# Optimization experiments

Hardware: AMD Instinct MI355X
Metric: run time of the kernel (lower is better)

## Reference

```python
import jax, jax.numpy as jnp
import numpy as np

EPS = 1e-6

def _layernorm2d(x, w, b):
    # normalize over channel dim (axis=1) per (b,h,w)
    u = jnp.mean(x, axis=1, keepdims=True)
    s = jnp.mean((x - u) ** 2, axis=1, keepdims=True)
    xn = (x - u) / jnp.sqrt(s + EPS)
    return xn * w[None, :, None, None] + b[None, :, None, None]

def _conv1x1(x, w, b):
    # w: (O, C, 1, 1)
    y = jnp.einsum('bchw,oc->bohw', x, w[:, :, 0, 0])
    return y + b[None, :, None, None]

def _dwconv3x3(x, w):
    # w: (C, 1, 3, 3), groups = C, padding 1, no bias
    C = x.shape[1]
    return jax.lax.conv_general_dilated(
        x, w, window_strides=(1, 1), padding=((1, 1), (1, 1)),
        dimension_numbers=('NCHW', 'OIHW', 'NCHW'), feature_group_count=C)

def _linrec_scan(a, u, axis):
    # s_t = a_t * s_{t-1} + u_t via associative scan
    def comb(l, r):
        al, ul = l
        ar, ur = r
        return al * ar, ar * ul + ur
    return jax.lax.associative_scan(comb, (a, u), axis=axis)[1]

def _bidir_scan(z, a, b, g, axis):
    u = b * z
    s_f = _linrec_scan(a, u, axis)
    s_b = jnp.flip(_linrec_scan(jnp.flip(a, axis), jnp.flip(u, axis), axis), axis)
    return g * (s_f + s_b)

def setup_inputs() -> dict:
    key = jax.random.key(0)
    ks = jax.random.split(key, 6)
    B, C, H, W = 8, 192, 128, 128
    x = jax.random.normal(ks[0], (B, C, H, W), dtype=jnp.float32)
    ln_w = jnp.ones((C,), jnp.float32)
    ln_b = jnp.zeros((C,), jnp.float32)
    dw_w = jax.random.normal(ks[1], (C, 1, 3, 3), jnp.float32) * (1.0 / 3.0)
    loc_w = jax.random.normal(ks[2], (C, C, 1, 1), jnp.float32) * (1.0 / np.sqrt(C))
    loc_b = jnp.zeros((C,), jnp.float32)
    par_w = jax.random.normal(ks[3], (3 * C, C, 1, 1), jnp.float32) * (1.0 / np.sqrt(C))
    par_b = jnp.zeros((3 * C,), jnp.float32)
    out_w = jax.random.normal(ks[4], (C, C, 1, 1), jnp.float32) * (1.0 / np.sqrt(C))
    out_b = jnp.zeros((C,), jnp.float32)
    return {"x": x, "ln_w": ln_w, "ln_b": ln_b, "dw_w": dw_w,
            "loc_w": loc_w, "loc_b": loc_b, "par_w": par_w, "par_b": par_b,
            "out_w": out_w, "out_b": out_b}

def reference(x, ln_w, ln_b, dw_w, loc_w, loc_b, par_w, par_b, out_w, out_b):
    C = x.shape[1]
    z = _layernorm2d(x, ln_w, ln_b)
    local_feat = _conv1x1(_dwconv3x3(z, dw_w), loc_w, loc_b)
    gates = _conv1x1(z, par_w, par_b)
    alpha = jax.nn.sigmoid(gates[:, :C])
    beta = jax.nn.sigmoid(gates[:, C:2 * C])
    gamma = jax.nn.sigmoid(gates[:, 2 * C:])
    y_w = _bidir_scan(z, alpha, beta, gamma, axis=3)  # along W
    y_h = _bidir_scan(z, alpha, beta, gamma, axis=2)  # along H
    y = local_feat + 0.5 * (y_w + y_h)
    y = jax.nn.silu(y)
    y = _conv1x1(y, out_w, out_b)
    return x + y
```

## Files before the change

### kernel.cpp

```cpp
#include <hip/hip_runtime.h>
#include <cstdint>
#include <cstddef>

#define B 8
#define C 192
#define H 128
#define W 128
#define HW (H * W)
#define CHW ((size_t)C * HW)
#define K C

typedef __attribute__((ext_vector_type(8))) short short8v;
typedef __attribute__((ext_vector_type(4))) float f32x4;
typedef __attribute__((ext_vector_type(4))) unsigned short ushort4v;

__device__ __forceinline__ float bf2f(unsigned short s) {
    union { float f; unsigned u; } cv; cv.u = ((unsigned)s) << 16; return cv.f;
}
__device__ __forceinline__ unsigned short f2bf(float f) {
    union { float f; unsigned u; } cv; cv.f = f;
    unsigned r = (cv.u + 0x7fffu + ((cv.u >> 16) & 1u)) >> 16;
    return (unsigned short)r;
}

__global__ void prepack_kernel(const float* __restrict__ pw, const float* __restrict__ lw,
                               const float* __restrict__ ow, unsigned short* __restrict__ wb) {
    int i = blockIdx.x * 256 + threadIdx.x;
    const int NPW = 3 * C * K, NL = C * K;
    if (i < NPW) wb[i] = f2bf(pw[i]);
    else if (i < NPW + NL) wb[i] = f2bf(lw[i - NPW]);
    else if (i < NPW + 2 * NL) wb[i] = f2bf(ow[i - NPW - NL]);
}

__global__ void ln_kernel(const float* __restrict__ x, const float* __restrict__ lw,
                          const float* __restrict__ lb, unsigned short* __restrict__ zt,
                          unsigned short* __restrict__ zn) {
    int p = blockIdx.x * 256 + threadIdx.x;
    int b = p >> 14, hw = p & 16383;
    const float* xp = x + (size_t)b * CHW + hw;
    float sum = 0.f, sq = 0.f;
    for (int c = 0; c < C; ++c) {
        float v = xp[(size_t)c * HW];
        sum += v; sq += v * v;
    }
    float mean = sum * (1.0f / C);
    float var = fmaxf(sq * (1.0f / C) - mean * mean, 0.f);
    float rs = rsqrtf(var + 1e-6f);
    unsigned short* zp = zt + (size_t)p * K;
    unsigned short* znp = zn + (size_t)b * CHW + hw;
#pragma unroll 4
    for (int c8 = 0; c8 < K / 8; ++c8) {
        short8v v;
#pragma unroll
        for (int j = 0; j < 8; ++j) {
            int c = c8 * 8 + j;
            float r = (xp[(size_t)c * HW] - mean) * rs * lw[c] + lb[c];
            unsigned short rb = f2bf(r);
            v[j] = (short)rb;
            znp[(size_t)c * HW] = rb;
        }
        *(short8v*)(zp + c8 * 8) = v;
    }
}

template <int MODE>
__global__ __launch_bounds__(256, 4)
void conv_mfma_kernel(const unsigned short* __restrict__ zt, const unsigned short* __restrict__ yin,
                      const unsigned short* __restrict__ zn,
                      const unsigned short* __restrict__ wb, const float* __restrict__ bias,
                      const float* __restrict__ xres, float* __restrict__ Pf,
                      unsigned short* __restrict__ PA, unsigned short* __restrict__ PU,
                      unsigned short* __restrict__ PG) {
    __shared__ char smem[96 * 384];
    int tid = threadIdx.x;
    int lane = tid & 63, wv = tid >> 6;
    int p0 = blockIdx.x * 128 + wv * 32;
    int lr = lane & 15, lh = lane >> 4;
    int sw = (lr & 7) << 4;

    short8v bfr[2][6];
    if (MODE != 2) {
#pragma unroll
        for (int s = 0; s < 2; ++s) {
            const unsigned short* zr = zt + (size_t)(p0 + s * 16 + lr) * K + lh * 8;
#pragma unroll
            for (int t = 0; t < 6; ++t) bfr[s][t] = *(const short8v*)(zr + t * 32);
        }
    } else {
        int bl = p0 >> 14, hwb = p0 & 16383;
        const unsigned short* yb = yin + (size_t)bl * CHW;
#pragma unroll
        for (int s = 0; s < 2; ++s) {
            int hw = hwb + s * 16 + lr;
#pragma unroll
            for (int t = 0; t < 6; ++t) {
                int c0 = t * 32 + lh * 8;
                short8v v;
#pragma unroll
                for (int j = 0; j < 8; ++j)
                    v[j] = (short)yb[(size_t)(c0 + j) * HW + hw];
                bfr[s][t] = v;
            }
        }
    }

    const int NGY = (MODE == 0) ? 3 : 1;
    for (int gy = 0; gy < NGY; ++gy) {
        for (int hf = 0; hf < 2; ++hf) {
            __syncthreads();
            const unsigned short* wsrc = wb + (size_t)gy * C * K + (size_t)hf * 96 * K;
#pragma unroll
            for (int it = 0; it < 9; ++it) {
                int e8 = it * 256 + tid;
                int row = e8 / 24;
                int cb = (e8 % 24) * 16;
                short8v v = *(const short8v*)(wsrc + e8 * 8);
                *(short8v*)(smem + row * 384 + (cb ^ ((row & 7) << 4))) = v;
            }
            __syncthreads();

            for (int otl = 0; otl < 6; ++otl) {
                int ot = hf * 6 + otl;
                int rb = (otl * 16 + lr) * 384;
                int o = ot * 16 + lr;
                f32x4 acc[2];
#pragma unroll
                for (int s = 0; s < 2; ++s) acc[s] = (f32x4){0.f, 0.f, 0.f, 0.f};
#pragma unroll
                for (int t = 0; t < 6; ++t) {
                    short8v af = *(const short8v*)(smem + rb + ((t * 64 + lh * 16) ^ sw));
#pragma unroll
                    for (int s = 0; s < 2; ++s)
                        acc[s] = __builtin_amdgcn_mfma_f32_16x16x32_bf16(bfr[s][t], af, acc[s], 0, 0, 0);
                }
                float bi = bias[(MODE == 0 ? gy * C : 0) + o];
#pragma unroll
                for (int s = 0; s < 2; ++s) {
                    int pst = p0 + s * 16 + lh * 4;
                    int bl = pst >> 14, hw = pst & 16383;
                    if (MODE == 0) {
                        ushort4v q;
                        ushort4v z4;
                        if (gy == 1)
                            z4 = *(const ushort4v*)(zn + (size_t)bl * CHW + (size_t)o * HW + hw);
#pragma unroll
                        for (int j = 0; j < 4; ++j) {
                            float v = acc[s][j] + bi;
                            v = 1.f / (1.f + __expf(-v));
                            if (gy == 1) v *= bf2f(z4[j]);
                            q[j] = f2bf(v);
                        }
                        unsigned short* dst = (gy == 0) ? PA : ((gy == 1) ? PU : PG);
                        *(ushort4v*)(dst + (size_t)bl * CHW + (size_t)o * HW + hw) = q;
                    } else if (MODE == 1) {
                        ushort4v q;
#pragma unroll
                        for (int j = 0; j < 4; ++j) q[j] = f2bf(acc[s][j] + bi);
                        *(ushort4v*)(PA + (size_t)bl * CHW + (size_t)o * HW + hw) = q;
                    } else {
                        size_t ad = (size_t)bl * CHW + (size_t)o * HW + hw;
                        f32x4 x4 = *(const f32x4*)(xres + ad);
                        f32x4 q;
#pragma unroll
                        for (int j = 0; j < 4; ++j) q[j] = acc[s][j] + bi + x4[j];
                        *(f32x4*)(Pf + ad) = q;
                    }
                }
            }
        }
    }
}

#define TROWS 180
#define LPAD  392
__global__ __launch_bounds__(256, 2)
void dw3x3_kernel(const unsigned short* __restrict__ zt, const float* __restrict__ wgt,
                  unsigned short* __restrict__ dt) {
    __shared__ char lds[TROWS * LPAD];
    int tid = threadIdx.x;
    int bx = blockIdx.x;
    int bimg = bx >> 7;
    int rem = bx & 127;
    int th = rem >> 3, tw = rem & 7;
    int h0 = th * 8, w0 = tw * 16;
    size_t ibase = (size_t)bimg * HW;

    for (int e = tid; e < TROWS * 24; e += 256) {
        int row = e / 24, ch = e % 24;
        int hh = row / 18, ww = row % 18;
        int h = h0 - 1 + hh, w = w0 - 1 + ww;
        short8v v;
        if (h >= 0 && h < H && w >= 0 && w < W)
            v = *(const short8v*)(zt + (ibase + h * W + w) * K + ch * 8);
        else
            v = (short8v){0, 0, 0, 0, 0, 0, 0, 0};
        *(short8v*)(lds + row * LPAD + ch * 16) = v;
    }
    __syncthreads();

    int w_l = tid & 15, h_l = (tid >> 4) & 7, half = tid >> 7;
    int p_out = (h0 + h_l) * W + (w0 + w_l);
    unsigned short* dp = dt + (ibase + p_out) * K + half * 96;
#pragma unroll
    for (int cc = 0; cc < 12; ++cc) {
        int c8 = half * 12 + cc;
        float acc[8];
#pragma unroll
        for (int j = 0; j < 8; ++j) acc[j] = 0.f;
#pragma unroll
        for (int dy = -1; dy <= 1; ++dy) {
#pragma unroll
            for (int dx = -1; dx <= 1; ++dx) {
                int row = (h_l + 1 + dy) * 18 + (w_l + 1 + dx);
                short8v zv = *(const short8v*)(lds + row * LPAD + c8 * 16);
                int t = (dy + 1) * 3 + (dx + 1);
#pragma unroll
                for (int j = 0; j < 8; ++j)
                    acc[j] += wgt[(c8 * 8 + j) * 9 + t] * bf2f((unsigned short)zv[j]);
            }
        }
        short8v ov;
#pragma unroll
        for (int j = 0; j < 8; ++j) ov[j] = (short)f2bf(acc[j]);
        *(short8v*)(dp + cc * 8) = ov;
    }
}

__global__ __launch_bounds__(1024)
void scan_fused_kernel(const unsigned short* __restrict__ A_, const unsigned short* __restrict__ U_,
                       const unsigned short* __restrict__ G_, unsigned short* __restrict__ LY) {
    extern __shared__ float Sl[];
    float* AF = Sl + HW;
    float* UF = AF + 1024;
    float* AB = UF + 1024;
    float* UB = AB + 1024;
    int tid = threadIdx.x, lane = tid & 63, wvi = tid >> 6;
    size_t pb = (size_t)blockIdx.x * HW;

#pragma unroll
    for (int i = 0; i < 8; ++i) {
        int r = wvi * 8 + i;
        size_t base = pb + (size_t)r * W;
        ushort2 av = *(const ushort2*)(A_ + base + 2 * lane);
        ushort2 uv = *(const ushort2*)(U_ + base + 2 * lane);
        float a0 = bf2f(av.x), a1 = bf2f(av.y);
        float u0 = bf2f(uv.x), u1 = bf2f(uv.y);

        float Aa = a0 * a1;
        float Uu = a1 * u0 + u1;
#pragma unroll
        for (int d = 1; d < 64; d <<= 1) {
            float Ao = __shfl_up(Aa, (unsigned)d, 64);
            float Uo = __shfl_up(Uu, (unsigned)d, 64);
            if (lane >= d) { Uu = Aa * Uo + Uu; Aa = Aa * Ao; }
        }
        float sp = __shfl_up(Uu, 1u, 64);
        if (lane == 0) sp = 0.f;
        float s0 = a0 * sp + u0;
        float s1 = a1 * s0 + u1;

        Aa = a0 * a1;
        Uu = a0 * u1 + u0;
#pragma unroll
        for (int d = 1; d < 64; d <<= 1) {
            float Ao = __shfl_down(Aa, (unsigned)d, 64);
            float Uo = __shfl_down(Uu, (unsigned)d, 64);
            if (lane + d < 64) { Uu = Aa * Uo + Uu; Aa = Aa * Ao; }
        }
        float tn = __shfl_down(Uu, 1u, 64);
        if (lane == 63) tn = 0.f;
        float t1 = a1 * tn + u1;
        float t0 = a0 * t1 + u0;

        Sl[r * W + 2 * lane]     = s0 + t0;
        Sl[r * W + 2 * lane + 1] = s1 + t1;
    }

    int w = tid & 127, ck = tid >> 7;
    int h0 = ck * 16;
    float av[16], uv[16];
#pragma unroll
    for (int i = 0; i < 16; ++i) {
        size_t off = pb + (size_t)(h0 + i) * W + w;
        av[i] = bf2f(A_[off]);
        uv[i] = bf2f(U_[off]);
    }
    float Af = 1.f, Uf = 0.f, Ab = 1.f, Ub = 0.f;
#pragma unroll
    for (int i = 0; i < 16; ++i) { Uf = av[i] * Uf + uv[i]; Af *= av[i]; }
#pragma unroll
    for (int i = 15; i >= 0; --i) { Ub = av[i] * Ub + uv[i]; Ab *= av[i]; }
    AF[ck * 128 + w] = Af; UF[ck * 128 + w] = Uf;
    AB[ck * 128 + w] = Ab; UB[ck * 128 + w] = Ub;
    __syncthreads();

    if (tid < 128) {
        float s = 0.f;
#pragma unroll
        for (int k = 0; k < 8; ++k) {
            float Aa = AF[k * 128 + tid], Uu = UF[k * 128 + tid];
            UF[k * 128 + tid] = s;
            s = Aa * s + Uu;
        }
    } else if (tid < 256) {
        int ww = tid - 128;
        float s = 0.f;
#pragma unroll
        for (int k = 7; k >= 0; --k) {
            float Aa = AB[k * 128 + ww], Uu = UB[k * 128 + ww];
            UB[k * 128 + ww] = s;
            s = Aa * s + Uu;
        }
    }
    __syncthreads();

    float sf = UF[ck * 128 + w];
    float sfa[16];
#pragma unroll
    for (int i = 0; i < 16; ++i) { sf = av[i] * sf + uv[i]; sfa[i] = sf; }
    float sb = UB[ck * 128 + w];
#pragma unroll
    for (int i = 15; i >= 0; --i) {
        sb = av[i] * sb + uv[i];
        size_t off = pb + (size_t)(h0 + i) * W + w;
        float g = bf2f(G_[off]);
        float v = bf2f(LY[off]) + 0.5f * g * (Sl[(h0 + i) * W + w] + sfa[i] + sb);
        LY[off] = f2bf(v / (1.f + __expf(-v)));
    }
}

extern "C" void kernel_launch(void* const* d_in, const int* in_sizes, int n_in,
                              void* d_out, int out_size, void* d_ws, size_t ws_size,
                              hipStream_t stream) {
    const float* x     = (const float*)d_in[0];
    const float* ln_w  = (const float*)d_in[1];
    const float* ln_b  = (const float*)d_in[2];
    const float* dw_w  = (const float*)d_in[3];
    const float* loc_w = (const float*)d_in[4];
    const float* loc_b = (const float*)d_in[5];
    const float* par_w = (const float*)d_in[6];
    const float* par_b = (const float*)d_in[7];
    const float* out_w = (const float*)d_in[8];
    const float* out_b = (const float*)d_in[9];
    float* out = (float*)d_out;
    unsigned short* wsu = (unsigned short*)d_ws;

    const int WBN = 5 * C * K;
    int nb = 8;
    while (nb > 1) {
        size_t need = (size_t)WBN * 2 + (size_t)5 * nb * CHW * 2;
        if (need <= ws_size) break;
        nb >>= 1;
    }

    prepack_kernel<<<(WBN + 255) / 256, 256, 0, stream>>>(par_w, loc_w, out_w, wsu);

    for (int b0 = 0; b0 < B; b0 += nb) {
        size_t ge = (size_t)nb * CHW;
        unsigned short* WB = wsu;
        unsigned short* Ab = wsu + WBN;
        unsigned short* Ub = Ab + ge;
        unsigned short* Gb = Ub + ge;
        unsigned short* ZT = Gb + ge;
        unsigned short* DT = ZT + ge;
        const float* xg = x + (size_t)b0 * CHW;
        int npg = nb * HW;

        ln_kernel<<<npg / 256, 256, 0, stream>>>(xg, ln_w, ln_b, ZT, DT);
        conv_mfma_kernel<0><<<npg / 128, 256, 0, stream>>>(
            ZT, nullptr, DT, WB, par_b, nullptr, nullptr, Ab, Ub, Gb);
        dw3x3_kernel<<<nb * 128, 256, 0, stream>>>(ZT, dw_w, DT);
        conv_mfma_kernel<1><<<npg / 128, 256, 0, stream>>>(
            DT, nullptr, nullptr, WB + 3 * C * K, loc_b, nullptr, nullptr, ZT, nullptr, nullptr);
        scan_fused_kernel<<<nb * C, 1024, (HW + 4096) * 4, stream>>>(Ab, Ub, Gb, ZT);
        conv_mfma_kernel<2><<<npg / 128, 256, 0, stream>>>(
            nullptr, ZT, nullptr, WB + 4 * C * K, out_b, xg, out + (size_t)b0 * CHW,
            nullptr, nullptr, nullptr);
    }
}
```

Measured before the change: 385.8 us.

## Stage A/U plane in swizzled LDS and replace wave-shuffle W-scan with chunked scan

The scan kernel now loads each A/U plane from global memory once, using wide vector loads. It packs the two values into a swizzled LDS buffer and reuses that buffer for the H-direction scan instead of re-reading global memory. The W-direction scan drops the 64-lane shuffle Hillis-Steele scan in favour of the same chunked serial-plus-carry scheme used for H, with padded carry arrays to avoid bank conflicts. This cuts global traffic and shuffle work, but adds two extra barriers and about 64 KB more LDS per block, which may limit occupancy.

```diff
diff --git a/kernel.cpp b/kernel.cpp
--- a/kernel.cpp
+++ b/kernel.cpp
@@ -229,77 +229,119 @@
 __global__ __launch_bounds__(1024)
 void scan_fused_kernel(const unsigned short* __restrict__ A_, const unsigned short* __restrict__ U_,
                        const unsigned short* __restrict__ G_, unsigned short* __restrict__ LY) {
-    extern __shared__ float Sl[];
-    float* AF = Sl + HW;
-    float* UF = AF + 1024;
-    float* AB = UF + 1024;
-    float* UB = AB + 1024;
-    int tid = threadIdx.x, lane = tid & 63, wvi = tid >> 6;
+    extern __shared__ float SMEM[];
+    float* Sl = SMEM;
+    unsigned* AU = (unsigned*)(SMEM + HW);
+    float* CA = SMEM + 2 * HW;
+    float* CU = CA + 1056;
+    float* DA = CU + 1056;
+    float* DU = DA + 1056;
+    int tid = threadIdx.x;
     size_t pb = (size_t)blockIdx.x * HW;
 
-#pragma unroll
-    for (int i = 0; i < 8; ++i) {
-        int r = wvi * 8 + i;
-        size_t base = pb + (size_t)r * W;
-        ushort2 av = *(const ushort2*)(A_ + base + 2 * lane);
-        ushort2 uv = *(const ushort2*)(U_ + base + 2 * lane);
-        float a0 = bf2f(av.x), a1 = bf2f(av.y);
-        float u0 = bf2f(uv.x), u1 = bf2f(uv.y);
-
-        float Aa = a0 * a1;
-        float Uu = a1 * u0 + u1;
-#pragma unroll
-        for (int d = 1; d < 64; d <<= 1) {
-            float Ao = __shfl_up(Aa, (unsigned)d, 64);
-            float Uo = __shfl_up(Uu, (unsigned)d, 64);
-            if (lane >= d) { Uu = Aa * Uo + Uu; Aa = Aa * Ao; }
-        }
-        float sp = __shfl_up(Uu, 1u, 64);
-        if (lane == 0) sp = 0.f;
-        float s0 = a0 * sp + u0;
-        float s1 = a1 * s0 + u1;
-
-        Aa = a0 * a1;
-        Uu = a0 * u1 + u0;
-#pragma unroll
-        for (int d = 1; d < 64; d <<= 1) {
-            float Ao = __shfl_down(Aa, (unsigned)d, 64);
-            float Uo = __shfl_down(Uu, (unsigned)d, 64);
-            if (lane + d < 64) { Uu = Aa * Uo + Uu; Aa = Aa * Ao; }
-        }
-        float tn = __shfl_down(Uu, 1u, 64);
-        if (lane == 63) tn = 0.f;
-        float t1 = a1 * tn + u1;
-        float t0 = a0 * t1 + u0;
-
-        Sl[r * W + 2 * lane]     = s0 + t0;
-        Sl[r * W + 2 * lane + 1] = s1 + t1;
-    }
-
-    int w = tid & 127, ck = tid >> 7;
-    int h0 = ck * 16;
-    float av[16], uv[16];
-#pragma unroll
-    for (int i = 0; i < 16; ++i) {
-        size_t off = pb + (size_t)(h0 + i) * W + w;
-        av[i] = bf2f(A_[off]);
-        uv[i] = bf2f(U_[off]);
-    }
-    float Af = 1.f, Uf = 0.f, Ab = 1.f, Ub = 0.f;
-#pragma unroll
-    for (int i = 0; i < 16; ++i) { Uf = av[i] * Uf + uv[i]; Af *= av[i]; }
-#pragma unroll
-    for (int i = 15; i >= 0; --i) { Ub = av[i] * Ub + uv[i]; Ab *= av[i]; }
-    AF[ck * 128 + w] = Af; UF[ck * 128 + w] = Uf;
-    AB[ck * 128 + w] = Ab; UB[ck * 128 + w] = Ub;
+    int h = tid >> 3, wc = tid & 7;
+    int swzA = (h & 7) << 2;
+    unsigned au[16];
+    {
+        const unsigned short* ap = A_ + pb + h * W + wc * 16;
+        const unsigned short* up = U_ + pb + h * W + wc * 16;
+        short8v a0 = *(const short8v*)ap, a1 = *(const short8v*)(ap + 8);
+        short8v u0 = *(const short8v*)up, u1 = *(const short8v*)(up + 8);
+#pragma unroll
+        for (int i = 0; i < 8; ++i) {
+            au[i]     = (unsigned)(unsigned short)a0[i] | ((unsigned)(unsigned short)u0[i] << 16);
+            au[8 + i] = (unsigned)(unsigned short)a1[i] | ((unsigned)(unsigned short)u1[i] << 16);
+        }
+    }
+#pragma unroll
+    for (int i = 0; i < 16; ++i)
+        AU[h * 128 + ((wc * 16 + i) ^ swzA)] = au[i];
+    {
+        float Af = 1.f, Uf = 0.f, Ab = 1.f, Ub = 0.f;
+#pragma unroll
+        for (int i = 0; i < 16; ++i) {
+            float a = bf2f(au[i] & 0xffff), u = bf2f(au[i] >> 16);
+            Uf = a * Uf + u; Af *= a;
+        }
+#pragma unroll
+        for (int i = 15; i >= 0; --i) {
+            float a = bf2f(au[i] & 0xffff), u = bf2f(au[i] >> 16);
+            Ub = a * Ub + u; Ab *= a;
+        }
+        CA[wc * 132 + h] = Af; CU[wc * 132 + h] = Uf;
+        DA[wc * 132 + h] = Ab; DU[wc * 132 + h] = Ub;
+    }
     __syncthreads();
 
     if (tid < 128) {
         float s = 0.f;
 #pragma unroll
         for (int k = 0; k < 8; ++k) {
-            float Aa = AF[k * 128 + tid], Uu = UF[k * 128 + tid];
-            UF[k * 128 + tid] = s;
+            float Aa = CA[k * 132 + tid], Uu = CU[k * 132 + tid];
+            CU[k * 132 + tid] = s;
+            s = Aa * s + Uu;
+        }
+    } else if (tid < 256) {
+        int hh = tid - 128;
+        float s = 0.f;
+#pragma unroll
+        for (int k = 7; k >= 0; --k) {
+            float Aa = DA[k * 132 + hh], Uu = DU[k * 132 + hh];
+            DU[k * 132 + hh] = s;
+            s = Aa * s + Uu;
+        }
+    }
+    __syncthreads();
+
+    {
+        float sf = CU[wc * 132 + h];
+        float sfa[16];
+#pragma unroll
+        for (int i = 0; i < 16; ++i) {
+            float a = bf2f(au[i] & 0xffff), u = bf2f(au[i] >> 16);
+            sf = a * sf + u; sfa[i] = sf;
+        }
+        float sb = DU[wc * 132 + h];
+#pragma unroll
+        for (int i = 15; i >= 0; --i) {
+            float a = bf2f(au[i] & 0xffff), u = bf2f(au[i] >> 16);
+            sb = a * sb + u;
+            Sl[h * W + ((wc * 16 + i) ^ swzA)] = sfa[i] + sb;
+        }
+    }
+    __syncthreads();
+
+    int w = tid & 127, hc = tid >> 7;
+    int h0 = hc * 16;
+    unsigned au2[16];
+#pragma unroll
+    for (int i = 0; i < 16; ++i) {
+        int hh = h0 + i;
+        au2[i] = AU[hh * 128 + (w ^ ((hh & 7) << 2))];
+    }
+    {
+        float Af = 1.f, Uf = 0.f, Ab = 1.f, Ub = 0.f;
+#pragma unroll
+        for (int i = 0; i < 16; ++i) {
+            float a = bf2f(au2[i] & 0xffff), u = bf2f(au2[i] >> 16);
+            Uf = a * Uf + u; Af *= a;
+        }
+#pragma unroll
+        for (int i = 15; i >= 0; --i) {
+            float a = bf2f(au2[i] & 0xffff), u = bf2f(au2[i] >> 16);
+            Ub = a * Ub + u; Ab *= a;
+        }
+        CA[hc * 132 + w] = Af; CU[hc * 132 + w] = Uf;
+        DA[hc * 132 + w] = Ab; DU[hc * 132 + w] = Ub;
+    }
+    __syncthreads();
+
+    if (tid < 128) {
+        float s = 0.f;
+#pragma unroll
+        for (int k = 0; k < 8; ++k) {
+            float Aa = CA[k * 132 + tid], Uu = CU[k * 132 + tid];
+            CU[k * 132 + tid] = s;
             s = Aa * s + Uu;
         }
     } else if (tid < 256) {
@@ -307,25 +349,33 @@
         float s = 0.f;
 #pragma unroll
         for (int k = 7; k >= 0; --k) {
-            float Aa = AB[k * 128 + ww], Uu = UB[k * 128 + ww];
-            UB[k * 128 + ww] = s;
+            float Aa = DA[k * 132 + ww], Uu = DU[k * 132 + ww];
+            DU[k * 132 + ww] = s;
             s = Aa * s + Uu;
         }
     }
     __syncthreads();
 
-    float sf = UF[ck * 128 + w];
-    float sfa[16];
-#pragma unroll
-    for (int i = 0; i < 16; ++i) { sf = av[i] * sf + uv[i]; sfa[i] = sf; }
-    float sb = UB[ck * 128 + w];
-#pragma unroll
-    for (int i = 15; i >= 0; --i) {
-        sb = av[i] * sb + uv[i];
-        size_t off = pb + (size_t)(h0 + i) * W + w;
-        float g = bf2f(G_[off]);
-        float v = bf2f(LY[off]) + 0.5f * g * (Sl[(h0 + i) * W + w] + sfa[i] + sb);
-        LY[off] = f2bf(v / (1.f + __expf(-v)));
+    {
+        float sf = CU[hc * 132 + w];
+        float sfa[16];
+#pragma unroll
+        for (int i = 0; i < 16; ++i) {
+            float a = bf2f(au2[i] & 0xffff), u = bf2f(au2[i] >> 16);
+            sf = a * sf + u; sfa[i] = sf;
+        }
+        float sb = DU[hc * 132 + w];
+#pragma unroll
+        for (int i = 15; i >= 0; --i) {
+            float a = bf2f(au2[i] & 0xffff), u = bf2f(au2[i] >> 16);
+            sb = a * sb + u;
+            int hh = h0 + i;
+            size_t off = pb + (size_t)hh * W + w;
+            float g = bf2f(G_[off]);
+            float wsum = Sl[hh * W + (w ^ ((hh & 7) << 2))];
+            float v = bf2f(LY[off]) + 0.5f * g * (wsum + sfa[i] + sb);
+            LY[off] = f2bf(v / (1.f + __expf(-v)));
+        }
     }
 }
 
@@ -355,6 +405,8 @@
 
     prepack_kernel<<<(WBN + 255) / 256, 256, 0, stream>>>(par_w, loc_w, out_w, wsu);
 
+    const size_t SCAN_LDS = (size_t)(2 * HW + 4 * 1056) * 4;
+
     for (int b0 = 0; b0 < B; b0 += nb) {
         size_t ge = (size_t)nb * CHW;
         unsigned short* WB = wsu;
@@ -372,7 +424,7 @@
         dw3x3_kernel<<<nb * 128, 256, 0, stream>>>(ZT, dw_w, DT);
         conv_mfma_kernel<1><<<npg / 128, 256, 0, stream>>>(
             DT, nullptr, nullptr, WB + 3 * C * K, loc_b, nullptr, nullptr, ZT, nullptr, nullptr);
-        scan_fused_kernel<<<nb * C, 1024, (HW + 4096) * 4, stream>>>(Ab, Ub, Gb, ZT);
+        scan_fused_kernel<<<nb * C, 1024, SCAN_LDS, stream>>>(Ab, Ub, Gb, ZT);
         conv_mfma_kernel<2><<<npg / 128, 256, 0, stream>>>(
             nullptr, ZT, nullptr, WB + 4 * C * K, out_b, xg, out + (size_t)b0 * CHW,
             nullptr, nullptr, nullptr);
```

Result: faster. 358.0 us (-7.2%).
